# Performance work log

Measured on AMD Instinct MI355X. Metric: run time of the kernel, lower is better.

The kernel has to match this reference:

```python
import jax, jax.numpy as jnp
import numpy as np

DIM = 512
HEADS = 8
DIM_HEAD = 64
INNER = HEADS * DIM_HEAD  # 512
HIDDEN = 512 * 4          # mlp_dim * expansion
EPS = 1e-5
SCALE = DIM_HEAD ** -0.5


def layernorm(x, w, b):
    mu = jnp.mean(x, axis=-1, keepdims=True)
    var = jnp.var(x, axis=-1, keepdims=True)
    return (x - mu) * jax.lax.rsqrt(var + EPS) * w + b


def setup_inputs() -> dict:
    key = jax.random.key(0)
    ks = jax.random.split(key, 12)
    B, P, N = 2, 8, 1024  # P must equal HEADS (axis-swap bug in original rearrange)
    s = lambda k, shape, fan: jax.random.normal(k, shape, jnp.float32) * (fan ** -0.5)
    return {
        "x": jax.random.normal(ks[0], (B, P, N, DIM), jnp.float32),
        "ln0_w": jnp.ones((DIM,), jnp.float32),
        "ln0_b": jnp.zeros((DIM,), jnp.float32),
        "ln1_w": jnp.ones((DIM,), jnp.float32),
        "ln1_b": jnp.zeros((DIM,), jnp.float32),
        "w_qkv": s(ks[1], (DIM, 3 * INNER), DIM),
        "w_o": s(ks[2], (INNER, DIM), INNER),
        "b_o": jnp.zeros((DIM,), jnp.float32),
        "w1": s(ks[3], (DIM, HIDDEN), DIM),
        "b1": jnp.zeros((HIDDEN,), jnp.float32),
        "w2": s(ks[4], (HIDDEN, DIM), HIDDEN),
        "b2": jnp.zeros((DIM,), jnp.float32),
    }


def reference(x, ln0_w, ln0_b, ln1_w, ln1_b, w_qkv, w_o, b_o, w1, b1, w2, b2):
    B, P, N, _ = x.shape
    x = layernorm(x, ln0_w, ln0_b)  # outer block norm

    # ---- VisionAttention ----
    h = layernorm(x, ln1_w, ln1_b)
    qkv = h @ w_qkv                                    # [B,P,N,3*INNER]
    q, k, v = jnp.split(qkv, 3, axis=-1)
    def to_heads(t):  # [B,P,N,H*D] -> [B,H,P,N,D]
        return t.reshape(B, P, N, HEADS, DIM_HEAD).transpose(0, 3, 1, 2, 4)
    q, k, v = to_heads(q), to_heads(k), to_heads(v)
    dots = jnp.einsum("bhpnd,bhpmd->bhpnm", q, k) * SCALE  # full NxN scores
    attn = jax.nn.softmax(dots, axis=-1)
    out = jnp.einsum("bhpnm,bhpmd->bhpnd", attn, v)        # [B,H,P,N,D]
    # Faithful to buggy rearrange 'b p h n d -> b p n (h d)': swaps H and P axes.
    out = out.transpose(0, 1, 3, 2, 4).reshape(B, HEADS, N, P * DIM_HEAD)
    out = out @ w_o + b_o                                  # [B,H,N,DIM]
    x = out + x  # residual (valid because P == HEADS)

    # ---- MLP ----
    m = jax.nn.gelu(x @ w1 + b1, approximate=False) @ w2 + b2
    return m + x
```

## Files before the change

### kernel.cpp

```cpp
#include <hip/hip_runtime.h>
#include <hip/hip_bf16.h>
#include <math.h>

#define DIMV 512
#define NTOK 16384
#define NSEQ 1024
#define HEADSV 8
#define PPV 8
#define DHEAD 64
#define QKVW 1536
#define HIDV 2048
#define SC2 0.18033688011112042f

typedef unsigned short ushort;
typedef unsigned int uint;
typedef __attribute__((ext_vector_type(8))) short short8;
typedef __attribute__((ext_vector_type(8))) unsigned short ushort8;
typedef __attribute__((ext_vector_type(4))) unsigned short ushortx4;
typedef __attribute__((ext_vector_type(4))) float floatx4;

__device__ __forceinline__ float bf2f(ushort u){
  union { unsigned int i; float f; } c; c.i = ((unsigned int)u) << 16; return c.f;
}
__device__ __forceinline__ ushort f2bf(float f){
  union { float f; unsigned int i; } c; c.f = f;
  unsigned int u = c.i + 0x7fffu + ((c.i >> 16) & 1u);
  return (ushort)(u >> 16);
}
__device__ __forceinline__ void async_copy16(const void* gptr, void* lptr){
  __builtin_amdgcn_global_load_lds((const __attribute__((address_space(1))) void*)gptr,
                                   (__attribute__((address_space(3))) void*)lptr, 16, 0, 0);
}
__device__ __forceinline__ float fast_gelu(float x){
  float u = x * (2.3022084f + 0.1029435f * x * x);
  return x * __builtin_amdgcn_rcpf(1.f + exp2f(-u));
}

__device__ __forceinline__ void wave_reduce2(float& a, float& b){
  #pragma unroll
  for (int off = 32; off > 0; off >>= 1){
    a += __shfl_down(a, off, 64);
    b += __shfl_down(b, off, 64);
  }
}

__device__ __forceinline__ void wtrans_body(const float* __restrict__ W,
    __hip_bfloat16* __restrict__ Wt, int K, int N, int bx, int by, int t,
    float* tile ){
  int bn = bx * 32, bk = by * 32;
  int tx = t & 31, ty = t >> 5;
  #pragma unroll
  for (int i = 0; i < 32; i += 8)
    tile[(ty + i) * 33 + tx] = W[(size_t)(bk + ty + i) * N + bn + tx];
  __syncthreads();
  #pragma unroll
  for (int i = 0; i < 32; i += 8)
    Wt[(size_t)(bn + ty + i) * K + bk + tx] = __float2bfloat16(tile[tx * 33 + ty + i]);
}

__global__ __launch_bounds__(256) void prep_kernel(const float* __restrict__ x,
    const float* __restrict__ w0, const float* __restrict__ b0,
    const float* __restrict__ w1ln, const float* __restrict__ b1ln,
    __hip_bfloat16* __restrict__ x1, __hip_bfloat16* __restrict__ h,
    const float* __restrict__ wqkv, __hip_bfloat16* __restrict__ wqkvT,
    const float* __restrict__ wo,   __hip_bfloat16* __restrict__ woT,
    const float* __restrict__ w1,   __hip_bfloat16* __restrict__ w1T,
    const float* __restrict__ w2,   __hip_bfloat16* __restrict__ w2T){
  __shared__ float smem[32 * 33];
  int bid = blockIdx.x;
  int t = threadIdx.x;
  if (bid >= NTOK){
    int r = bid - NTOK;
    if (r < 768)        wtrans_body(wqkv, wqkvT, 512, 1536, r % 48, r / 48, t, smem);
    else if (r < 1024){ r -= 768;  wtrans_body(wo, woT, 512, 512,  r % 16, r / 16, t, smem); }
    else if (r < 2048){ r -= 1024; wtrans_body(w1, w1T, 512, 2048, r % 64, r / 64, t, smem); }
    else             { r -= 2048; wtrans_body(w2, w2T, 2048, 512, r % 16, r / 16, t, smem); }
    return;
  }
  float* sm = smem;
  size_t row = bid;
  const float2* xr = (const float2*)(x + row * DIMV);
  float2 v = xr[t];
  float s = v.x + v.y;
  float sq = v.x * v.x + v.y * v.y;
  wave_reduce2(s, sq);
  int wid = t >> 6, lane = t & 63;
  if (lane == 0){ sm[wid] = s; sm[8 + wid] = sq; }
  __syncthreads();
  s  = sm[0] + sm[1] + sm[2] + sm[3];
  sq = sm[8] + sm[9] + sm[10] + sm[11];
  float mu = s * (1.f / DIMV);
  float var = sq * (1.f / DIMV) - mu * mu;
  float r = rsqrtf(var + 1e-5f);
  float2 ww = ((const float2*)w0)[t];
  float2 bb = ((const float2*)b0)[t];
  float2 y;
  y.x = (v.x - mu) * r * ww.x + bb.x;
  y.y = (v.y - mu) * r * ww.y + bb.y;
  ushort2 xb; xb.x = f2bf(y.x); xb.y = f2bf(y.y);
  ((ushort2*)(x1 + row * DIMV))[t] = xb;
  float s2 = y.x + y.y, sq2 = y.x * y.x + y.y * y.y;
  wave_reduce2(s2, sq2);
  __syncthreads();
  if (lane == 0){ sm[wid] = s2; sm[8 + wid] = sq2; }
  __syncthreads();
  s2  = sm[0] + sm[1] + sm[2] + sm[3];
  sq2 = sm[8] + sm[9] + sm[10] + sm[11];
  float mu2 = s2 * (1.f / DIMV);
  float var2 = sq2 * (1.f / DIMV) - mu2 * mu2;
  float r2 = rsqrtf(var2 + 1e-5f);
  float2 w1v = ((const float2*)w1ln)[t];
  float2 b1v = ((const float2*)b1ln)[t];
  float hx = (y.x - mu2) * r2 * w1v.x + b1v.x;
  float hy = (y.y - mu2) * r2 * w1v.y + b1v.y;
  ushort2 hb; hb.x = f2bf(hx); hb.y = f2bf(hy);
  ((ushort2*)(h + row * DIMV))[t] = hb;
}

template<int SWAP>
__global__ __launch_bounds__(512, 2) void gemm_8p(
    const __hip_bfloat16* __restrict__ A,
    const __hip_bfloat16* __restrict__ Bt,
    const float* __restrict__ bias,
    __hip_bfloat16* __restrict__ Cb,
    ushort* __restrict__ vt,
    int M, int N, int K, int gx, int dogelu)
{
  __shared__ __hip_bfloat16 As[2][256 * 64];
  __shared__ __hip_bfloat16 Bs[2][256 * 64];
  int tid = threadIdx.x;
  int l = tid & 63, w = tid >> 6;
  int wr = w >> 2, wc = w & 3;
  int fm = l & 15, quad = l >> 4;

  int bid = blockIdx.x;
  int xcd = bid & 7, idx = bid >> 3;
  int xl = idx % gx, yl = idx / gx;
  size_t bm = (size_t)(xcd * 8 + yl) * 256;
  size_t bn = (size_t)xl * 256;

  int sr = tid >> 3;
  int sc = ((tid & 7) ^ (sr & 7)) * 8;
  const __hip_bfloat16* Ab0 = A + (bm + sr) * (size_t)K + sc;
  const __hip_bfloat16* Bb0 = Bt + (bn + sr) * (size_t)K + sc;
  int ldst = tid * 8;

  int nk = K >> 6;

  #pragma unroll
  for (int j = 0; j < 4; j++)
    async_copy16(Ab0 + (size_t)j * 64 * K, &As[0][j * 4096 + ldst]);
  #pragma unroll
  for (int j = 0; j < 4; j++)
    async_copy16(Bb0 + (size_t)j * 64 * K, &Bs[0][j * 4096 + ldst]);

  floatx4 acc[8][4] = {};

  int arow = wr * 128 + fm;
  int brow = wc * 64 + fm;
  int cx = fm & 7;

  for (int t = 0; t < nk; ++t){
    int cur = t & 1, nxt = cur ^ 1;
    asm volatile("s_waitcnt vmcnt(0)\n\ts_barrier" ::: "memory");
    if (t + 1 < nk){
      const __hip_bfloat16* Asrc = Ab0 + (size_t)(t + 1) * 64;
      const __hip_bfloat16* Bsrc = Bb0 + (size_t)(t + 1) * 64;
      #pragma unroll
      for (int j = 0; j < 4; j++)
        async_copy16(Asrc + (size_t)j * 64 * K, &As[nxt][j * 4096 + ldst]);
      #pragma unroll
      for (int j = 0; j < 4; j++)
        async_copy16(Bsrc + (size_t)j * 64 * K, &Bs[nxt][j * 4096 + ldst]);
    }
    const __hip_bfloat16* Ac = As[cur];
    const __hip_bfloat16* Bc = Bs[cur];
    short8 bf[4][2];
    #pragma unroll
    for (int ci = 0; ci < 4; ci++)
      #pragma unroll
      for (int kb = 0; kb < 2; kb++)
        bf[ci][kb] = *(const short8*)&Bc[(brow + ci * 16) * 64 + ((kb * 4 + quad) ^ cx) * 8];
    #pragma unroll
    for (int p = 0; p < 4; p++){
      short8 af[2][2];
      #pragma unroll
      for (int i = 0; i < 2; i++)
        #pragma unroll
        for (int kb = 0; kb < 2; kb++)
          af[i][kb] = *(const short8*)&Ac[(arow + (p * 2 + i) * 16) * 64 + ((kb * 4 + quad) ^ cx) * 8];
      #pragma unroll
      for (int i = 0; i < 2; i++)
        #pragma unroll
        for (int ci = 0; ci < 4; ci++)
          #pragma unroll
          for (int kb = 0; kb < 2; kb++){
            if (SWAP)
              acc[p * 2 + i][ci] = __builtin_amdgcn_mfma_f32_16x16x32_bf16(bf[ci][kb], af[i][kb], acc[p * 2 + i][ci], 0, 0, 0);
            else
              acc[p * 2 + i][ci] = __builtin_amdgcn_mfma_f32_16x16x32_bf16(af[i][kb], bf[ci][kb], acc[p * 2 + i][ci], 0, 0, 0);
          }
      if (p == 1)
        asm volatile("s_barrier" ::: "memory");
    }
  }

  if (SWAP){
    #pragma unroll
    for (int ri = 0; ri < 8; ri++){
      size_t row = bm + wr * 128 + ri * 16 + fm;
      size_t rbase = row * (size_t)N + bn + wc * 64 + quad * 4;
      #pragma unroll
      for (int ci = 0; ci < 4; ci++){
        floatx4 v = acc[ri][ci];
        if (bias){
          floatx4 bv = *(const floatx4*)(bias + bn + wc * 64 + ci * 16 + quad * 4);
          #pragma unroll
          for (int r2 = 0; r2 < 4; r2++) v[r2] += bv[r2];
        }
        if (dogelu){
          #pragma unroll
          for (int r2 = 0; r2 < 4; r2++) v[r2] = fast_gelu(v[r2]);
        }
        ushortx4 ob;
        #pragma unroll
        for (int r2 = 0; r2 < 4; r2++) ob[r2] = f2bf(v[r2]);
        *(ushortx4*)((ushort*)Cb + rbase + ci * 16) = ob;
      }
    }
  } else {
    int b = (int)(bm >> 13), p = (int)((bm >> 10) & 7);
    int n0 = (int)(bm & 1023) + wr * 128 + quad * 4;
    #pragma unroll
    for (int ci = 0; ci < 4; ci++){
      int col = (int)bn + wc * 64 + ci * 16 + fm;
      if (col >= 1024){
        int cc = col - 1024, hh = cc >> 6, dd = cc & 63;
        ushort* vdst = vt + ((size_t)((b * 8 + hh) * 8 + p)) * 65536 + (size_t)dd * 1024 + n0;
        #pragma unroll
        for (int ri = 0; ri < 8; ri++){
          ushortx4 v4;
          v4[0] = f2bf(acc[ri][ci][0]); v4[1] = f2bf(acc[ri][ci][1]);
          v4[2] = f2bf(acc[ri][ci][2]); v4[3] = f2bf(acc[ri][ci][3]);
          *(ushortx4*)(vdst + ri * 16) = v4;
        }
      } else {
        float scl = (col < 512) ? SC2 : 1.f;
        #pragma unroll
        for (int ri = 0; ri < 8; ri++){
          size_t rowb = bm + wr * 128 + ri * 16 + quad * 4;
          #pragma unroll
          for (int r2 = 0; r2 < 4; r2++)
            ((ushort*)Cb)[(rowb + r2) * (size_t)N + col] = f2bf(acc[ri][ci][r2] * scl);
        }
      }
    }
  }
}

template<int SWAP>
__global__ __launch_bounds__(256) void gemm_mfma(
    const __hip_bfloat16* __restrict__ A,
    const __hip_bfloat16* __restrict__ Bt,
    const float* __restrict__ bias,
    const __hip_bfloat16* __restrict__ Rb,
    float* __restrict__ Cf,
    __hip_bfloat16* __restrict__ Cb,
    ushort* __restrict__ vt,
    int M, int N, int K, int gx, int dogelu)
{
  __shared__ __hip_bfloat16 As[3][128 * 32];
  __shared__ __hip_bfloat16 Bs[3][128 * 32];
  int tid = threadIdx.x;
  int w = tid >> 6, l = tid & 63;

  int bid = blockIdx.x;
  int xcd = bid & 7, idx = bid >> 3;
  int xl = idx % gx, yl = idx / gx;
  size_t bm = (size_t)(xcd * 16 + yl) * 128;
  size_t bn = (size_t)xl * 128;
  int wm = (w & 1) * 64, wn = (w >> 1) * 64;

  int srow = w * 16 + (l >> 2);
  int gcs = ((l & 3) ^ (srow & 3)) * 8;
  const __hip_bfloat16* Ag0 = A + (bm + srow) * K + gcs;
  const __hip_bfloat16* Ag1 = A + (bm + 64 + srow) * K + gcs;
  const __hip_bfloat16* Bg0 = Bt + (bn + srow) * K + gcs;
  const __hip_bfloat16* Bg1 = Bt + (bn + 64 + srow) * K + gcs;
  int lo = srow * 32 + (l & 3) * 8;

  floatx4 acc[4][4] = {};
  int fm = l & 15;
  int quad = l >> 4;
  int cs = fm & 3;

  int nk = K >> 5;
  async_copy16(Ag0, &As[0][lo]);
  async_copy16(Ag1, &As[0][lo + 64 * 32]);
  async_copy16(Bg0, &Bs[0][lo]);
  async_copy16(Bg1, &Bs[0][lo + 64 * 32]);
  if (nk > 1){
    async_copy16(Ag0 + 32, &As[1][lo]);
    async_copy16(Ag1 + 32, &As[1][lo + 64 * 32]);
    async_copy16(Bg0 + 32, &Bs[1][lo]);
    async_copy16(Bg1 + 32, &Bs[1][lo + 64 * 32]);
  }

  int rb = 0;
  for (int it = 0; it < nk; ++it){
    if (it + 1 < nk)
      asm volatile("s_waitcnt vmcnt(4)\n\ts_barrier" ::: "memory");
    else
      asm volatile("s_waitcnt vmcnt(0)\n\ts_barrier" ::: "memory");
    if (it + 2 < nk){
      int wb = rb >= 1 ? rb - 1 : 2;
      int k0 = (it + 2) << 5;
      async_copy16(Ag0 + k0, &As[wb][lo]);
      async_copy16(Ag1 + k0, &As[wb][lo + 64 * 32]);
      async_copy16(Bg0 + k0, &Bs[wb][lo]);
      async_copy16(Bg1 + k0, &Bs[wb][lo + 64 * 32]);
    }
    const __hip_bfloat16* Ab = As[rb];
    const __hip_bfloat16* Bb = Bs[rb];
    short8 af[4], bf[4];
    #pragma unroll
    for (int i = 0; i < 4; i++){
      af[i] = *(const short8*)&Ab[(wm + i * 16 + fm) * 32 + ((quad ^ cs) * 8)];
      bf[i] = *(const short8*)&Bb[(wn + i * 16 + fm) * 32 + ((quad ^ cs) * 8)];
    }
    #pragma unroll
    for (int mi = 0; mi < 4; mi++)
      #pragma unroll
      for (int ni = 0; ni < 4; ni++){
        if (SWAP)
          acc[mi][ni] = __builtin_amdgcn_mfma_f32_16x16x32_bf16(bf[ni], af[mi], acc[mi][ni], 0, 0, 0);
        else
          acc[mi][ni] = __builtin_amdgcn_mfma_f32_16x16x32_bf16(af[mi], bf[ni], acc[mi][ni], 0, 0, 0);
      }
    rb = rb < 2 ? rb + 1 : 0;
  }

  int rq = quad * 4;
  if (SWAP){
    #pragma unroll
    for (int mi = 0; mi < 4; mi++){
      size_t row = bm + wm + mi * 16 + fm;
      size_t rbase = row * (size_t)N + bn + wn + rq;
      #pragma unroll
      for (int ni = 0; ni < 4; ni++){
        size_t idx2 = rbase + ni * 16;
        floatx4 v = acc[mi][ni];
        if (bias){
          floatx4 bv = *(const floatx4*)(bias + bn + wn + ni * 16 + rq);
          #pragma unroll
          for (int r2 = 0; r2 < 4; r2++) v[r2] += bv[r2];
        }
        if (dogelu){
          #pragma unroll
          for (int r2 = 0; r2 < 4; r2++) v[r2] = fast_gelu(v[r2]);
        }
        if (Rb){
          ushortx4 rbv = *(const ushortx4*)((const ushort*)Rb + idx2);
          #pragma unroll
          for (int r2 = 0; r2 < 4; r2++) v[r2] += bf2f(rbv[r2]);
        }
        if (Cb){
          ushortx4 ob;
          #pragma unroll
          for (int r2 = 0; r2 < 4; r2++) ob[r2] = f2bf(v[r2]);
          *(ushortx4*)((ushort*)Cb + idx2) = ob;
        } else {
          *(floatx4*)(Cf + idx2) = v;
        }
      }
    }
  } else {
    #pragma unroll
    for (int ni = 0; ni < 4; ni++){
      size_t col = bn + wn + ni * 16 + fm;
      float bv = bias ? bias[col] : 0.f;
      #pragma unroll
      for (int mi = 0; mi < 4; mi++){
        #pragma unroll
        for (int r2 = 0; r2 < 4; r2++){
          size_t row = bm + wm + mi * 16 + rq + r2;
          float v = acc[mi][ni][r2] + bv;
          if (dogelu) v = fast_gelu(v);
          size_t idx2 = row * N + col;
          if (Rb) v += bf2f(((const ushort*)Rb)[idx2]);
          Cf[idx2] = v;
        }
      }
    }
  }
}

__global__ __launch_bounds__(256, 4) void attn_mfma(const __hip_bfloat16* __restrict__ qkvp,
                                                    const ushort* __restrict__ vt,
                                                    __hip_bfloat16* __restrict__ outp){
  __shared__ ushort Ks[2][64 * 64];
  __shared__ ushort Vs[2][64 * 64];
  __shared__ ushort Ps[4][32 * 32];
  int tid = threadIdx.x;
  int w = tid >> 6, l = tid & 63;
  int r15 = l & 15, quad = l >> 4, fq = quad * 8;
  int slice = blockIdx.x & 127;
  int qc = blockIdx.x >> 7;
  int b = slice >> 6, hh = (slice >> 3) & 7, p = slice & 7;
  const ushort* base = (const ushort*)qkvp + (size_t)(b * PPV + p) * NSEQ * QKVW;
  const ushort* kb = base + 512 + hh * DHEAD;
  const ushort* vb = vt + (size_t)slice * 65536;

  int s0 = w * 64 + l, s1 = 256 + w * 64 + l;
  int row0 = s0 >> 3, row1 = s1 >> 3;
  int gc0 = (s0 & 7) ^ (row0 & 7), gc1 = (s1 & 7) ^ (row1 & 7);
  const ushort* kp0 = kb + (size_t)row0 * QKVW + gc0 * 8;
  const ushort* kp1 = kb + (size_t)row1 * QKVW + gc1 * 8;
  const ushort* vp0 = vb + (size_t)row0 * 1024 + gc0 * 8;
  const ushort* vp1 = vb + (size_t)row1 * 1024 + gc1 * 8;

  async_copy16(kp0, &Ks[0][s0 * 8]);
  async_copy16(kp1, &Ks[0][s1 * 8]);
  async_copy16(vp0, &Vs[0][s0 * 8]);
  async_copy16(vp1, &Vs[0][s1 * 8]);

  int q0 = qc * 128 + w * 32;
  short8 qf[2][2];
  #pragma unroll
  for (int mi = 0; mi < 2; mi++)
    #pragma unroll
    for (int kk = 0; kk < 2; kk++)
      qf[mi][kk] = *(const short8*)(base + (size_t)(q0 + mi * 16 + r15) * QKVW + hh * DHEAD + kk * 32 + fq);

  floatx4 o[2][4] = {};
  floatx4 lacc[2] = {};
  short8 ones;
  #pragma unroll
  for (int j = 0; j < 8; j++) ones[j] = (short)0x3F80;

  int sw = r15 & 7;
  int swp = (r15 & 3) << 3;
  ushort* PsW = Ps[w];

  for (int it = 0; it < NSEQ / 64; ++it){
    int cur = it & 1;
    asm volatile("s_waitcnt vmcnt(0)\n\ts_barrier" ::: "memory");
    if (it + 1 < NSEQ / 64){
      int nxt = cur ^ 1;
      kp0 += 64 * QKVW; kp1 += 64 * QKVW; vp0 += 64; vp1 += 64;
      async_copy16(kp0, &Ks[nxt][s0 * 8]);
      async_copy16(kp1, &Ks[nxt][s1 * 8]);
      async_copy16(vp0, &Vs[nxt][s0 * 8]);
      async_copy16(vp1, &Vs[nxt][s1 * 8]);
    }
    const ushort* Kb = Ks[cur];
    const ushort* Vb = Vs[cur];

    short8 pf[2][2];
    #pragma unroll
    for (int kk = 0; kk < 2; kk++){
      #pragma unroll
      for (int nn = 0; nn < 2; nn++){
        int ni = kk * 2 + nn;
        int rb2 = (ni * 16 + r15) * 64;
        short8 kf0 = *(const short8*)&Kb[rb2 + (quad ^ sw) * 8];
        short8 kf1 = *(const short8*)&Kb[rb2 + ((4 + quad) ^ sw) * 8];
        floatx4 sA = {}, sB = {};
        sA = __builtin_amdgcn_mfma_f32_16x16x32_bf16(kf0, qf[0][0], sA, 0, 0, 0);
        sA = __builtin_amdgcn_mfma_f32_16x16x32_bf16(kf1, qf[0][1], sA, 0, 0, 0);
        sB = __builtin_amdgcn_mfma_f32_16x16x32_bf16(kf0, qf[1][0], sB, 0, 0, 0);
        sB = __builtin_amdgcn_mfma_f32_16x16x32_bf16(kf1, qf[1][1], sB, 0, 0, 0);
        int wc = (nn * 16 + quad * 4) ^ swp;
        union { float f; uint u; } e0, e1, e2, e3;
        uint2 pk;
        e0.f = exp2f(sA[0]); e1.f = exp2f(sA[1]);
        e2.f = exp2f(sA[2]); e3.f = exp2f(sA[3]);
        pk.x = __builtin_amdgcn_perm(e1.u, e0.u, 0x07060302u);
        pk.y = __builtin_amdgcn_perm(e3.u, e2.u, 0x07060302u);
        *(uint2*)&PsW[r15 * 32 + wc] = pk;
        e0.f = exp2f(sB[0]); e1.f = exp2f(sB[1]);
        e2.f = exp2f(sB[2]); e3.f = exp2f(sB[3]);
        pk.x = __builtin_amdgcn_perm(e1.u, e0.u, 0x07060302u);
        pk.y = __builtin_amdgcn_perm(e3.u, e2.u, 0x07060302u);
        *(uint2*)&PsW[(16 + r15) * 32 + wc] = pk;
      }
      asm volatile("s_waitcnt lgkmcnt(0)" ::: "memory");
      pf[0][kk] = *(const short8*)&PsW[r15 * 32 + (fq ^ swp)];
      pf[1][kk] = *(const short8*)&PsW[(16 + r15) * 32 + (fq ^ swp)];
      asm volatile("s_waitcnt lgkmcnt(0)" ::: "memory");
    }

    #pragma unroll
    for (int mi = 0; mi < 2; mi++)
      #pragma unroll
      for (int kk = 0; kk < 2; kk++)
        lacc[mi] = __builtin_amdgcn_mfma_f32_16x16x32_bf16(ones, pf[mi][kk], lacc[mi], 0, 0, 0);

    #pragma unroll
    for (int dj = 0; dj < 4; dj++){
      int d = dj * 16 + r15;
      short8 vf0 = *(const short8*)&Vb[d * 64 + ((quad) ^ sw) * 8];
      short8 vf1 = *(const short8*)&Vb[d * 64 + ((4 + quad) ^ sw) * 8];
      #pragma unroll
      for (int mi = 0; mi < 2; mi++){
        o[mi][dj] = __builtin_amdgcn_mfma_f32_16x16x32_bf16(vf0, pf[mi][0], o[mi][dj], 0, 0, 0);
        o[mi][dj] = __builtin_amdgcn_mfma_f32_16x16x32_bf16(vf1, pf[mi][1], o[mi][dj], 0, 0, 0);
      }
    }
  }

  #pragma unroll
  for (int mi = 0; mi < 2; mi++){
    float inv = __builtin_amdgcn_rcpf(lacc[mi][0]);
    size_t n = q0 + mi * 16 + r15;
    ushort* orow = (ushort*)outp + ((size_t)((b * HEADSV + hh) * NSEQ + n)) * DIMV + p * DHEAD + quad * 4;
    #pragma unroll
    for (int dj = 0; dj < 4; dj++){
      ushortx4 ov;
      #pragma unroll
      for (int r = 0; r < 4; r++) ov[r] = f2bf(o[mi][dj][r] * inv);
      *(ushortx4*)(orow + dj * 16) = ov;
    }
  }
}

extern "C" void kernel_launch(void* const* d_in, const int* in_sizes, int n_in,
                              void* d_out, int out_size, void* d_ws, size_t ws_size,
                              hipStream_t stream){
  (void)in_sizes; (void)n_in; (void)out_size; (void)ws_size;
  const float* x    = (const float*)d_in[0];
  const float* lw0  = (const float*)d_in[1];
  const float* lb0  = (const float*)d_in[2];
  const float* lw1  = (const float*)d_in[3];
  const float* lb1  = (const float*)d_in[4];
  const float* wqkv = (const float*)d_in[5];
  const float* wo   = (const float*)d_in[6];
  const float* bo   = (const float*)d_in[7];
  const float* w1   = (const float*)d_in[8];
  const float* b1   = (const float*)d_in[9];
  const float* w2   = (const float*)d_in[10];
  const float* b2   = (const float*)d_in[11];
  float* out = (float*)d_out;
  char* ws = (char*)d_ws;
  const size_t MB = 1024 * 1024;

  __hip_bfloat16* x1b  = (__hip_bfloat16*)(ws);
  ushort* vtbuf        = (ushort*)(ws + 32 * MB);
  __hip_bfloat16* x2b  = (__hip_bfloat16*)(ws + 64 * MB);
  __hip_bfloat16* wqkvT= (__hip_bfloat16*)(ws + 80 * MB);
  __hip_bfloat16* woT  = (__hip_bfloat16*)(ws + 82 * MB);
  __hip_bfloat16* w1T  = (__hip_bfloat16*)(ws + 83 * MB);
  __hip_bfloat16* w2T  = (__hip_bfloat16*)(ws + 85 * MB);
  __hip_bfloat16* hB   = (__hip_bfloat16*)(ws + 88 * MB);
  __hip_bfloat16* attnB= hB;
  __hip_bfloat16* qkvB = (__hip_bfloat16*)(ws + 104 * MB);
  __hip_bfloat16* tB   = (__hip_bfloat16*)(ws + 88 * MB);

  prep_kernel<<<NTOK + 3072, 256, 0, stream>>>(
      x, lw0, lb0, lw1, lb1, x1b, hB,
      wqkv, wqkvT, wo, woT, w1, w1T, w2, w2T);

  gemm_8p<0><<<384, 512, 0, stream>>>(
      hB, wqkvT, nullptr, qkvB, vtbuf, NTOK, QKVW, DIMV, 6, 0);

  attn_mfma<<<1024, 256, 0, stream>>>(qkvB, vtbuf, attnB);

  gemm_mfma<1><<<(DIMV / 128) * 128, 256, 0, stream>>>(
      attnB, woT, bo, x1b, nullptr, x2b, nullptr,
      NTOK, DIMV, DIMV, DIMV / 128, 0);

  gemm_8p<1><<<512, 512, 0, stream>>>(
      x2b, w1T, b1, tB, nullptr, NTOK, HIDV, DIMV, 8, 1);

  gemm_mfma<1><<<(DIMV / 128) * 128, 256, 0, stream>>>(
      tB, w2T, b2, x2b, out, nullptr, nullptr,
      NTOK, DIMV, HIDV, DIMV / 128, 0);
}
```

Measured before the change: 353.0 us.

## Process two rows per block in prep and double-buffer gemm_mfma for occupancy

The layernorm prep kernel now handles two token rows per 256-thread block with float4 loads and 4-wide bf16 stores, which halves the block count and widens memory accesses. gemm_mfma drops from a triple-buffered LDS pipeline with prefetch distance 2 to a double-buffered one with distance 1, and adds a launch bound of 4 blocks per CU. The goal is to cut LDS use and registers so more blocks fit on each CU. The risk is less latency hiding, since each iteration now waits with vmcnt(0) before issuing the next prefetch.

New measurement: 341.4 us. 3.3% less time.

```diff
diff --git a/kernel.cpp b/kernel.cpp
--- a/kernel.cpp
+++ b/kernel.cpp
@@ -69,8 +69,8 @@
   __shared__ float smem[32 * 33];
   int bid = blockIdx.x;
   int t = threadIdx.x;
-  if (bid >= NTOK){
-    int r = bid - NTOK;
+  if (bid >= NTOK / 2){
+    int r = bid - NTOK / 2;
     if (r < 768)        wtrans_body(wqkv, wqkvT, 512, 1536, r % 48, r / 48, t, smem);
     else if (r < 1024){ r -= 768;  wtrans_body(wo, woT, 512, 512,  r % 16, r / 16, t, smem); }
     else if (r < 2048){ r -= 1024; wtrans_body(w1, w1T, 512, 2048, r % 64, r / 64, t, smem); }
@@ -78,43 +78,50 @@
     return;
   }
   float* sm = smem;
-  size_t row = bid;
-  const float2* xr = (const float2*)(x + row * DIMV);
-  float2 v = xr[t];
-  float s = v.x + v.y;
-  float sq = v.x * v.x + v.y * v.y;
+  int rh = t >> 7;
+  int tc = t & 127;
+  size_t row = (size_t)bid * 2 + rh;
+  float4 v = ((const float4*)(x + row * DIMV))[tc];
+  float s = v.x + v.y + v.z + v.w;
+  float sq = v.x * v.x + v.y * v.y + v.z * v.z + v.w * v.w;
   wave_reduce2(s, sq);
   int wid = t >> 6, lane = t & 63;
   if (lane == 0){ sm[wid] = s; sm[8 + wid] = sq; }
   __syncthreads();
-  s  = sm[0] + sm[1] + sm[2] + sm[3];
-  sq = sm[8] + sm[9] + sm[10] + sm[11];
+  s  = sm[rh * 2] + sm[rh * 2 + 1];
+  sq = sm[8 + rh * 2] + sm[8 + rh * 2 + 1];
   float mu = s * (1.f / DIMV);
   float var = sq * (1.f / DIMV) - mu * mu;
   float r = rsqrtf(var + 1e-5f);
-  float2 ww = ((const float2*)w0)[t];
-  float2 bb = ((const float2*)b0)[t];
-  float2 y;
+  float4 ww = ((const float4*)w0)[tc];
+  float4 bb = ((const float4*)b0)[tc];
+  float4 y;
   y.x = (v.x - mu) * r * ww.x + bb.x;
   y.y = (v.y - mu) * r * ww.y + bb.y;
-  ushort2 xb; xb.x = f2bf(y.x); xb.y = f2bf(y.y);
-  ((ushort2*)(x1 + row * DIMV))[t] = xb;
-  float s2 = y.x + y.y, sq2 = y.x * y.x + y.y * y.y;
+  y.z = (v.z - mu) * r * ww.z + bb.z;
+  y.w = (v.w - mu) * r * ww.w + bb.w;
+  ushortx4 xb;
+  xb[0] = f2bf(y.x); xb[1] = f2bf(y.y); xb[2] = f2bf(y.z); xb[3] = f2bf(y.w);
+  *(ushortx4*)((ushort*)x1 + row * DIMV + tc * 4) = xb;
+  float s2 = y.x + y.y + y.z + y.w;
+  float sq2 = y.x * y.x + y.y * y.y + y.z * y.z + y.w * y.w;
   wave_reduce2(s2, sq2);
   __syncthreads();
   if (lane == 0){ sm[wid] = s2; sm[8 + wid] = sq2; }
   __syncthreads();
-  s2  = sm[0] + sm[1] + sm[2] + sm[3];
-  sq2 = sm[8] + sm[9] + sm[10] + sm[11];
+  s2  = sm[rh * 2] + sm[rh * 2 + 1];
+  sq2 = sm[8 + rh * 2] + sm[8 + rh * 2 + 1];
   float mu2 = s2 * (1.f / DIMV);
   float var2 = sq2 * (1.f / DIMV) - mu2 * mu2;
   float r2 = rsqrtf(var2 + 1e-5f);
-  float2 w1v = ((const float2*)w1ln)[t];
-  float2 b1v = ((const float2*)b1ln)[t];
-  float hx = (y.x - mu2) * r2 * w1v.x + b1v.x;
-  float hy = (y.y - mu2) * r2 * w1v.y + b1v.y;
-  ushort2 hb; hb.x = f2bf(hx); hb.y = f2bf(hy);
-  ((ushort2*)(h + row * DIMV))[t] = hb;
+  float4 w1v = ((const float4*)w1ln)[tc];
+  float4 b1v = ((const float4*)b1ln)[tc];
+  ushortx4 hb;
+  hb[0] = f2bf((y.x - mu2) * r2 * w1v.x + b1v.x);
+  hb[1] = f2bf((y.y - mu2) * r2 * w1v.y + b1v.y);
+  hb[2] = f2bf((y.z - mu2) * r2 * w1v.z + b1v.z);
+  hb[3] = f2bf((y.w - mu2) * r2 * w1v.w + b1v.w);
+  *(ushortx4*)((ushort*)h + row * DIMV + tc * 4) = hb;
 }
 
 template<int SWAP>
@@ -259,7 +266,7 @@
 }
 
 template<int SWAP>
-__global__ __launch_bounds__(256) void gemm_mfma(
+__global__ __launch_bounds__(256, 4) void gemm_mfma(
     const __hip_bfloat16* __restrict__ A,
     const __hip_bfloat16* __restrict__ Bt,
     const float* __restrict__ bias,
@@ -269,8 +276,8 @@
     ushort* __restrict__ vt,
     int M, int N, int K, int gx, int dogelu)
 {
-  __shared__ __hip_bfloat16 As[3][128 * 32];
-  __shared__ __hip_bfloat16 Bs[3][128 * 32];
+  __shared__ __hip_bfloat16 As[2][128 * 32];
+  __shared__ __hip_bfloat16 Bs[2][128 * 32];
   int tid = threadIdx.x;
   int w = tid >> 6, l = tid & 63;
 
@@ -299,29 +306,20 @@
   async_copy16(Ag1, &As[0][lo + 64 * 32]);
   async_copy16(Bg0, &Bs[0][lo]);
   async_copy16(Bg1, &Bs[0][lo + 64 * 32]);
-  if (nk > 1){
-    async_copy16(Ag0 + 32, &As[1][lo]);
-    async_copy16(Ag1 + 32, &As[1][lo + 64 * 32]);
-    async_copy16(Bg0 + 32, &Bs[1][lo]);
-    async_copy16(Bg1 + 32, &Bs[1][lo + 64 * 32]);
-  }
-
-  int rb = 0;
+
   for (int it = 0; it < nk; ++it){
-    if (it + 1 < nk)
-      asm volatile("s_waitcnt vmcnt(4)\n\ts_barrier" ::: "memory");
-    else
-      asm volatile("s_waitcnt vmcnt(0)\n\ts_barrier" ::: "memory");
-    if (it + 2 < nk){
-      int wb = rb >= 1 ? rb - 1 : 2;
-      int k0 = (it + 2) << 5;
-      async_copy16(Ag0 + k0, &As[wb][lo]);
-      async_copy16(Ag1 + k0, &As[wb][lo + 64 * 32]);
-      async_copy16(Bg0 + k0, &Bs[wb][lo]);
-      async_copy16(Bg1 + k0, &Bs[wb][lo + 64 * 32]);
-    }
-    const __hip_bfloat16* Ab = As[rb];
-    const __hip_bfloat16* Bb = Bs[rb];
+    int cur = it & 1;
+    asm volatile("s_waitcnt vmcnt(0)\n\ts_barrier" ::: "memory");
+    if (it + 1 < nk){
+      int nb = cur ^ 1;
+      int k0 = (it + 1) << 5;
+      async_copy16(Ag0 + k0, &As[nb][lo]);
+      async_copy16(Ag1 + k0, &As[nb][lo + 64 * 32]);
+      async_copy16(Bg0 + k0, &Bs[nb][lo]);
+      async_copy16(Bg1 + k0, &Bs[nb][lo + 64 * 32]);
+    }
+    const __hip_bfloat16* Ab = As[cur];
+    const __hip_bfloat16* Bb = Bs[cur];
     short8 af[4], bf[4];
     #pragma unroll
     for (int i = 0; i < 4; i++){
@@ -337,7 +335,6 @@
         else
           acc[mi][ni] = __builtin_amdgcn_mfma_f32_16x16x32_bf16(af[mi], bf[ni], acc[mi][ni], 0, 0, 0);
       }
-    rb = rb < 2 ? rb + 1 : 0;
   }
 
   int rq = quad * 4;
@@ -556,7 +553,7 @@
   __hip_bfloat16* qkvB = (__hip_bfloat16*)(ws + 104 * MB);
   __hip_bfloat16* tB   = (__hip_bfloat16*)(ws + 88 * MB);
 
-  prep_kernel<<<NTOK + 3072, 256, 0, stream>>>(
+  prep_kernel<<<NTOK / 2 + 3072, 256, 0, stream>>>(
       x, lw0, lb0, lw1, lb1, x1b, hB,
       wqkv, wqkvT, wo, woT, w1, w1T, w2, w2T);
 
```
